# Kernel tuning notes

Hardware: AMD Instinct MI355X
Metric: run time of the kernel (lower is better)

## Reference

```python
import jax, jax.numpy as jnp
import numpy as np

DIM = 2048
HEADS = 16
DIM_HEAD = 128
FF_INNER = DIM * 4
SCALE_BASE = 512
EPS = 1e-5


def setup_inputs() -> dict:
    key = jax.random.key(0)
    k1, k2, k3, k4 = jax.random.split(key, 4)
    fused_out = HEADS * DIM_HEAD + DIM_HEAD + DIM_HEAD + 2 * FF_INNER  # 18688
    x = jax.random.normal(k1, (2, 2048, DIM), dtype=jnp.float32)
    gamma = jnp.ones((DIM,), dtype=jnp.float32)
    W_fused = jax.random.normal(k2, (DIM, fused_out), dtype=jnp.float32) * 0.02
    W_attn_out = jax.random.normal(k3, (HEADS * DIM_HEAD, DIM), dtype=jnp.float32) * 0.02
    W_ff_out = jax.random.normal(k4, (FF_INNER, DIM), dtype=jnp.float32) * 0.02
    return {"x": x, "gamma": gamma, "W_fused": W_fused, "W_attn_out": W_attn_out, "W_ff_out": W_ff_out}


def _rotate_half(t):
    t1, t2 = jnp.split(t, 2, axis=-1)
    return jnp.concatenate((-t2, t1), axis=-1)


def _rotary(n, dtype):
    # RotaryEmbedding with use_xpos=True, scale_base=512
    half = DIM_HEAD // 2
    inv_freq = 1.0 / (10000.0 ** (jnp.arange(0, DIM_HEAD, 2, dtype=dtype) / DIM_HEAD))
    t = jnp.arange(n, dtype=dtype)
    freqs = jnp.einsum('i,j->ij', t, inv_freq)          # [n, half]
    freqs = jnp.concatenate((freqs, freqs), axis=-1)    # [n, dh]
    scale_vec = (jnp.arange(0, DIM_HEAD, 2, dtype=dtype) + 0.4 * DIM_HEAD) / (1.4 * DIM_HEAD)
    power = (t - n // 2) / SCALE_BASE
    scale = scale_vec[None, :] ** power[:, None]        # [n, half]
    scale = jnp.concatenate((scale, scale), axis=-1)    # [n, dh]
    return freqs, scale


def _apply_rope(pos, t, scale):
    return t * jnp.cos(pos) * scale + _rotate_half(t) * jnp.sin(pos) * scale


def reference(x, gamma, W_fused, W_attn_out, W_ff_out):
    b, n, d = x.shape
    # LayerNorm (beta fixed at zero)
    mu = jnp.mean(x, axis=-1, keepdims=True)
    var = jnp.var(x, axis=-1, keepdims=True)
    xn = (x - mu) * jax.lax.rsqrt(var + EPS) * gamma

    proj = xn @ W_fused
    attn_inner = HEADS * DIM_HEAD
    q = proj[..., :attn_inner]
    k = proj[..., attn_inner:attn_inner + DIM_HEAD]
    v = proj[..., attn_inner + DIM_HEAD:attn_inner + 2 * DIM_HEAD]
    ff = proj[..., attn_inner + 2 * DIM_HEAD:]

    q = q.reshape(b, n, HEADS, DIM_HEAD).transpose(0, 2, 1, 3)  # b h n d

    pos, scale = _rotary(n, x.dtype)
    q = _apply_rope(pos, q, scale)            # broadcasts [n,dh] over b,h
    k = _apply_rope(pos, k, 1.0 / scale)      # k is [b, n, dh]

    # multi-query attention, causal
    sim = jnp.einsum('bhid,bjd->bhij', q, k) * (DIM_HEAD ** -0.5)
    causal_mask = jnp.triu(jnp.ones((n, n), dtype=bool), 1)
    sim = jnp.where(causal_mask, jnp.finfo(sim.dtype).min, sim)
    attn = jax.nn.softmax(sim, axis=-1)
    out = jnp.einsum('bhij,bjd->bhid', attn, v)
    out = out.transpose(0, 2, 1, 3).reshape(b, n, attn_inner)
    attn_out = out @ W_attn_out

    # SwiGLU: chunk -> silu(gate) * x
    ff_x, ff_gate = jnp.split(ff, 2, axis=-1)
    ff_out = (jax.nn.silu(ff_gate) * ff_x) @ W_ff_out

    return attn_out + ff_out
```

## Files before the change

### kernel.cpp

```cpp
#include <hip/hip_runtime.h>

typedef __attribute__((ext_vector_type(8))) short short8;
typedef __attribute__((ext_vector_type(4))) float floatx4;
typedef __attribute__((ext_vector_type(8))) unsigned short ushort8;

#define FOUT 18688
#define FFI  8192
#define CATW 10240

__device__ __forceinline__ float b2f(unsigned short u){
  union { unsigned int i; float f; } v; v.i = ((unsigned int)u) << 16; return v.f;
}
__device__ __forceinline__ unsigned short f2b(float f){
  union { float f; unsigned int i; } v; v.f = f;
  unsigned int r = v.i + 0x7FFFu + ((v.i >> 16) & 1u);
  return (unsigned short)(r >> 16);
}
__device__ __forceinline__ void gld_lds16(const void* g, void* l){
  __builtin_amdgcn_global_load_lds((const __attribute__((address_space(1))) void*)g,
                                   (__attribute__((address_space(3))) void*)l, 16, 0, 0);
}

#define SCHED0() __builtin_amdgcn_sched_barrier(0)
#define BARR()   do{ SCHED0(); __builtin_amdgcn_s_barrier(); SCHED0(); }while(0)

__global__ __launch_bounds__(256) void ln_kernel(const float* __restrict__ x,
                                                 const float* __restrict__ gamma,
                                                 unsigned short* __restrict__ xn){
  int row = blockIdx.x;
  const float* xr = x + (size_t)row * 2048;
  int tid = threadIdx.x;
  float v[8]; float s = 0.f, s2 = 0.f;
#pragma unroll
  for(int i=0;i<8;i++){ float t = xr[tid + i*256]; v[i]=t; s+=t; s2+=t*t; }
#pragma unroll
  for(int off=32; off>=1; off>>=1){ s += __shfl_down(s, off, 64); s2 += __shfl_down(s2, off, 64); }
  __shared__ float red[8];
  int wv = tid>>6, ln_ = tid&63;
  if(ln_==0){ red[wv] = s; red[wv+4] = s2; }
  __syncthreads();
  s  = red[0]+red[1]+red[2]+red[3];
  s2 = red[4]+red[5]+red[6]+red[7];
  float mu  = s * (1.f/2048.f);
  float var = s2 * (1.f/2048.f) - mu*mu;
  float rstd = rsqrtf(var + 1e-5f);
#pragma unroll
  for(int i=0;i<8;i++){
    float o = (v[i]-mu)*rstd*gamma[tid + i*256];
    xn[(size_t)row*2048 + tid + i*256] = f2b(o);
  }
}

__global__ __launch_bounds__(256) void tcast64_kernel(const float* __restrict__ W,
                                                      unsigned short* __restrict__ Wt,
                                                      int C, int S, int O){
  __shared__ float t[64][65];
  int bx = blockIdx.x*64;
  int by = blockIdx.y*64;
  int tid = threadIdx.x;
  int r = tid>>2, cq = (tid&3)*16;
  const float* src = W + (size_t)(by + r)*C + bx + cq;
#pragma unroll
  for(int e=0;e<4;e++){
    floatx4 v = *(const floatx4*)(src + e*4);
    t[r][cq+e*4+0]=v[0]; t[r][cq+e*4+1]=v[1]; t[r][cq+e*4+2]=v[2]; t[r][cq+e*4+3]=v[3];
  }
  __syncthreads();
#pragma unroll
  for(int it=0; it<2; it++){
    int s_ = it*256 + tid;
    int c = s_>>3, j8 = s_&7;
    ushort8 o;
#pragma unroll
    for(int e=0;e<8;e++) o[e] = f2b(t[j8*8+e][c]);
    *(ushort8*)&Wt[(size_t)(bx+c)*S + O + by + j8*8] = o;
  }
}

__global__ void vtrans_kernel(const unsigned short* __restrict__ proj, unsigned short* __restrict__ vt){
  __shared__ unsigned short t[32][33];
  int b = blockIdx.z;
  int n0 = blockIdx.x*32, d0 = blockIdx.y*32;
  int tx = threadIdx.x, ty = threadIdx.y;
#pragma unroll
  for(int i=0;i<4;i++) t[ty+i*8][tx] = proj[(size_t)(b*2048 + n0+ty+i*8)*FOUT + 2176 + d0+tx];
  __syncthreads();
#pragma unroll
  for(int i=0;i<4;i++) vt[((size_t)b*128 + d0+ty+i*8)*2048 + n0+tx] = t[tx][ty+i*8];
}

__global__ __launch_bounds__(256) void rope_tab_kernel(floatx4* __restrict__ tab){
  int idx = blockIdx.x*256 + threadIdx.x;
  int i = idx >> 6, j = idx & 63;
  float fj = (float)j, fi = (float)i;
  float p = fi * powf(10000.f, -fj*(1.f/64.f));
  float c = cosf(p), s = sinf(p);
  float sv = (2.f*fj + 51.2f) * (1.f/179.2f);
  float pw = (fi - 1024.f) * (1.f/512.f);
  float sc = powf(sv, pw);
  const float att = 0.08838834764831843f;
  floatx4 o; o[0]=c*sc*att; o[1]=s*sc*att; o[2]=c/sc; o[3]=s/sc;
  tab[idx] = o;
}

__global__ __launch_bounds__(256) void rope_kernel(unsigned short* __restrict__ proj,
                                                   const floatx4* __restrict__ tab){
  int row = blockIdx.x;
  int i = row & 2047;
  unsigned short* pr = proj + (size_t)row*FOUT;
  for(int item = threadIdx.x; item < 17*64; item += 256){
    int slot = item >> 6;
    int j = item & 63;
    floatx4 t = tab[i*64 + j];
    float cs = (slot==16) ? t[2] : t[0];
    float ss = (slot==16) ? t[3] : t[1];
    int colbase = (slot<16) ? slot*128 : 2048;
    float x1 = b2f(pr[colbase+j]);
    float x2 = b2f(pr[colbase+j+64]);
    pr[colbase+j]    = f2b(x1*cs - x2*ss);
    pr[colbase+j+64] = f2b(x2*cs + x1*ss);
  }
}

template<int MODE>
__global__ __launch_bounds__(512, 2) void gemm8p_kernel(const unsigned short* __restrict__ A,
                                                        const unsigned short* __restrict__ Bt,
                                                        unsigned short* __restrict__ Cb,
                                                        float* __restrict__ Cf,
                                                        int N, int K, int NT, size_t zstride){
  __shared__ unsigned short lds[65536];
  const int tid = threadIdx.x;
  const int wave = tid>>6, lane = tid&63;
  const int l15 = lane&15, l4 = lane>>4;
  const int wr = wave>>2, wc = wave&3;
  int id = blockIdx.x;
  int cpx = (int)gridDim.x >> 3;
  int swz = (id & 7)*cpx + (id >> 3);
  int tm = swz & 15, tn = swz >> 4;
  int kbase = (int)blockIdx.z * (NT*64);
  const unsigned short* Ab = A  + (size_t)tm*256*K + kbase;
  const unsigned short* Bb = Bt + (size_t)tn*256*K + kbase;
  if(MODE==1) Cf += (size_t)blockIdx.z * zstride;

  const int r0 = tid>>3;
  const int colc = ((tid&7) ^ (r0&7))*8;
  const int dstw = wave*512;

#define STAGE(t_, h_, isB_) do{ \
    const unsigned short* g_ = (isB_) ? Bb : Ab; \
    int db_ = (((t_)&1)<<15) + ((isB_)<<14) + ((h_)<<13) + dstw; \
    gld_lds16(g_ + (size_t)((h_)*128 + r0)*K + (t_)*64 + colc, &lds[db_]); \
    gld_lds16(g_ + (size_t)((h_)*128 + r0 + 64)*K + (t_)*64 + colc, &lds[db_ + 4096]); \
  }while(0)

  const int sw8 = l15&7;
  const int fo0 = ((l4    )^sw8)*8;
  const int fo1 = ((l4 + 4)^sw8)*8;
  const int albase = (wr*128 + l15)*64;
  const int blbase = 16384 + (wc*64 + l15)*64;

#define RD_A4(arr_, buf_, mh_, fo_) do{ \
  _Pragma("unroll") for(int mf=0; mf<4; mf++) \
    arr_[mf] = *(const short8*)&lds[(buf_) + albase + (mh_)*4096 + mf*1024 + (fo_)]; }while(0)
#define RD_B4(arr_, buf_, fo_) do{ \
  _Pragma("unroll") for(int nf=0; nf<4; nf++) \
    arr_[nf] = *(const short8*)&lds[(buf_) + blbase + nf*1024 + (fo_)]; }while(0)
#define MFMA_P(aarr_, barr_, mh_) do{ \
  _Pragma("unroll") for(int mf=0; mf<4; mf++) \
  _Pragma("unroll") for(int nf=0; nf<4; nf++) \
    acc[(mh_)*4+mf][nf] = __builtin_amdgcn_mfma_f32_16x16x32_bf16( \
      aarr_[mf], barr_[nf], acc[(mh_)*4+mf][nf], 0,0,0); }while(0)

  floatx4 acc[8][4];
#pragma unroll
  for(int i=0;i<8;i++)
#pragma unroll
    for(int j=0;j<4;j++) acc[i][j] = (floatx4)0.f;

  STAGE(0,0,0); STAGE(0,1,0); STAGE(0,0,1); STAGE(0,1,1);
  STAGE(1,0,1); STAGE(1,1,1); STAGE(1,0,0);
  asm volatile("s_waitcnt vmcnt(6)" ::: "memory");
  BARR();

  short8 a00_[4], a01_[4], a10_[4], a11_[4], b0_[4], b1_[4];
  for(int t=0; t<NT; ++t){
    const int bufo = (t&1)<<15;
    RD_A4(a00_, bufo, 0, fo0);
    RD_B4(b0_,  bufo, fo0);
    if(t+1 < NT) STAGE(t+1,1,0);
    __builtin_amdgcn_s_setprio(1);
    MFMA_P(a00_, b0_, 0);
    __builtin_amdgcn_s_setprio(0);
    BARR();
    RD_A4(a01_, bufo, 0, fo1);
    RD_B4(b1_,  bufo, fo1);
    if(t+2 < NT) STAGE(t+2,0,1);
    __builtin_amdgcn_s_setprio(1);
    MFMA_P(a01_, b1_, 0);
    __builtin_amdgcn_s_setprio(0);
    BARR();
    RD_A4(a10_, bufo, 1, fo0);
    if(t+2 < NT) STAGE(t+2,1,1);
    __builtin_amdgcn_s_setprio(1);
    MFMA_P(a10_, b0_, 1);
    __builtin_amdgcn_s_setprio(0);
    BARR();
    RD_A4(a11_, bufo, 1, fo1);
    if(t+2 < NT){
      STAGE(t+2,0,0);
      asm volatile("s_waitcnt vmcnt(6)" ::: "memory");
    } else if(t+1 < NT){
      asm volatile("s_waitcnt vmcnt(0)" ::: "memory");
    }
    __builtin_amdgcn_s_setprio(1);
    MFMA_P(a11_, b1_, 1);
    __builtin_amdgcn_s_setprio(0);
    BARR();
  }

#pragma unroll
  for(int m=0;m<8;m++){
#pragma unroll
    for(int n=0;n<4;n++){
#pragma unroll
      for(int r=0;r<4;r++){
        size_t row = (size_t)tm*256 + wr*128 + (m>>2)*64 + (m&3)*16 + l4*4 + r;
        size_t col = (size_t)tn*256 + wc*64 + n*16 + l15;
        float v = acc[m][n][r];
        if(MODE==0)      Cb[row*N + col] = f2b(v);
        else             Cf[row*N + col] = v;
      }
    }
  }
}

__global__ __launch_bounds__(256) void add2_kernel(const float* __restrict__ p0,
                                                   const float* __restrict__ p1,
                                                   float* __restrict__ o, int n4){
  for(int i = blockIdx.x*256 + threadIdx.x; i < n4; i += gridDim.x*256){
    floatx4 a = ((const floatx4*)p0)[i];
    floatx4 b = ((const floatx4*)p1)[i];
    ((floatx4*)o)[i] = a + b;
  }
}

__global__ __launch_bounds__(512) void attn_kernel(const unsigned short* __restrict__ proj,
                                                   const unsigned short* __restrict__ vt,
                                                   unsigned short* __restrict__ ao){
  __shared__ unsigned short lK[64*128];
  __shared__ unsigned short lV[128*64];
  __shared__ unsigned short lP[8*16*64];
  int qt = (int)gridDim.x - 1 - (int)blockIdx.x;
  int hh = blockIdx.y, b = blockIdx.z;
  int tid = threadIdx.x, wave = tid>>6, lane = tid&63;
  int l15 = lane&15, l4 = lane>>4;
  int q0 = qt*128;
  int qrow = q0 + wave*16 + l15;
  const unsigned short* qp = proj + (size_t)(b*2048 + qrow)*FOUT + hh*128 + l4*8;
  short8 qf[4];
#pragma unroll
  for(int ds=0; ds<4; ds++) qf[ds] = *(const short8*)(qp + ds*32);
  floatx4 po[8];
#pragma unroll
  for(int dt=0; dt<8; dt++) po[dt] = (floatx4)0.f;
  float mrun[4] = {-1e30f,-1e30f,-1e30f,-1e30f};
  float lrun[4] = {0.f,0.f,0.f,0.f};
  unsigned short* lPw = lP + wave*1024;
  const unsigned short* kb = proj + (size_t)(b*2048)*FOUT + 2048;
  const unsigned short* vb = vt + (size_t)b*128*2048;
  int kvmax = 2*qt + 1;

  for(int kv=0; kv<=kvmax; kv++){
    int kv0 = kv*64;
#pragma unroll
    for(int it=0; it<2; it++){
      int f = it*512 + tid;
      int r = f>>4, pc = f&15;
      int gc = pc ^ (r&7);
      gld_lds16(kb + (size_t)(kv0 + r)*FOUT + gc*8, &lK[(it*512 + wave*64)*8]);
    }
#pragma unroll
    for(int it=0; it<2; it++){
      int f = it*512 + tid;
      int d = f>>3, pc = f&7;
      int gc = pc ^ (d&7);
      gld_lds16(vb + (size_t)d*2048 + kv0 + gc*8, &lV[(it*512 + wave*64)*8]);
    }
    __syncthreads();
    floatx4 sa[4];
#pragma unroll
    for(int jt=0;jt<4;jt++) sa[jt] = (floatx4)0.f;
#pragma unroll
    for(int jt=0;jt<4;jt++){
      int krow = jt*16 + l15;
#pragma unroll
      for(int ds=0; ds<4; ds++){
        int pc = (l4 + ds*4) ^ (krow&7);
        short8 kf = *(const short8*)&lK[krow*128 + pc*8];
        sa[jt] = __builtin_amdgcn_mfma_f32_16x16x32_bf16(qf[ds], kf, sa[jt], 0,0,0);
      }
    }
    float pv[4][4];
    bool diag = (kv0 + 63 > q0 + wave*16);
#pragma unroll
    for(int jt=0;jt<4;jt++){
#pragma unroll
      for(int r=0;r<4;r++){
        float s = sa[jt][r];
        if(diag && (kv0 + jt*16 + l15 > q0 + wave*16 + l4*4 + r)) s = -1e30f;
        pv[jt][r] = s;
      }
    }
    float mnew[4], corr[4];
#pragma unroll
    for(int r=0;r<4;r++){
      float mx = fmaxf(fmaxf(pv[0][r],pv[1][r]),fmaxf(pv[2][r],pv[3][r]));
      mx = fmaxf(mx, __shfl_xor(mx, 1, 64));
      mx = fmaxf(mx, __shfl_xor(mx, 2, 64));
      mx = fmaxf(mx, __shfl_xor(mx, 4, 64));
      mx = fmaxf(mx, __shfl_xor(mx, 8, 64));
      float mn = fmaxf(mrun[r], mx);
      corr[r] = __expf(mrun[r] - mn);
      mrun[r] = mn;
      mnew[r] = mn;
    }
    float rsum[4] = {0.f,0.f,0.f,0.f};
#pragma unroll
    for(int jt=0;jt<4;jt++){
#pragma unroll
      for(int r=0;r<4;r++){
        float p = __expf(pv[jt][r] - mnew[r]);
        pv[jt][r] = p;
        rsum[r] += p;
      }
    }
#pragma unroll
    for(int r=0;r<4;r++){
      float rs = rsum[r];
      rs += __shfl_xor(rs, 1, 64);
      rs += __shfl_xor(rs, 2, 64);
      rs += __shfl_xor(rs, 4, 64);
      rs += __shfl_xor(rs, 8, 64);
      lrun[r] = lrun[r]*corr[r] + rs;
    }
#pragma unroll
    for(int dt=0;dt<8;dt++){
#pragma unroll
      for(int r=0;r<4;r++) po[dt][r] *= corr[r];
    }
#pragma unroll
    for(int jt=0;jt<4;jt++){
#pragma unroll
      for(int r=0;r<4;r++){
        int i_ = l4*4 + r;
        int j = jt*16 + l15;
        int pc = (j>>3) ^ (i_&7);
        lPw[i_*64 + pc*8 + (j&7)] = f2b(pv[jt][r]);
      }
    }
    asm volatile("s_waitcnt lgkmcnt(0)" ::: "memory");
    short8 pf[2];
#pragma unroll
    for(int ks=0;ks<2;ks++){
      int pc = (l4 + ks*4) ^ (l15&7);
      pf[ks] = *(const short8*)&lPw[l15*64 + pc*8];
    }
#pragma unroll
    for(int dt=0;dt<8;dt++){
      int d = dt*16 + l15;
#pragma unroll
      for(int ks=0;ks<2;ks++){
        int pc = (ks*4 + l4) ^ (d&7);
        short8 vf = *(const short8*)&lV[d*64 + pc*8];
        po[dt] = __builtin_amdgcn_mfma_f32_16x16x32_bf16(pf[ks], vf, po[dt], 0,0,0);
      }
    }
    __syncthreads();
  }
#pragma unroll
  for(int r=0;r<4;r++){
    float inv = 1.f / lrun[r];
    size_t orow = (size_t)(b*2048 + q0 + wave*16 + l4*4 + r);
#pragma unroll
    for(int dt=0;dt<8;dt++){
      ao[orow*CATW + hh*128 + dt*16 + l15] = f2b(po[dt][r]*inv);
    }
  }
}

__global__ __launch_bounds__(256) void swiglu_kernel(const unsigned short* __restrict__ proj,
                                                     unsigned short* __restrict__ cat){
  size_t idx = (size_t)blockIdx.x*256 + threadIdx.x;
  int row = (int)(idx >> 10);
  int c8  = (int)(idx & 1023);
  const unsigned short* pr = proj + (size_t)row*FOUT + 2304 + c8*8;
  ushort8 xv = *(const ushort8*)pr;
  ushort8 gv = *(const ushort8*)(pr + FFI);
  ushort8 ov;
#pragma unroll
  for(int e=0;e<8;e++){
    float xf = b2f(xv[e]);
    float gf = b2f(gv[e]);
    float sg = gf / (1.f + __expf(-gf));
    ov[e] = f2b(sg*xf);
  }
  *(ushort8*)(cat + (size_t)row*CATW + 2048 + c8*8) = ov;
}

extern "C" void kernel_launch(void* const* d_in, const int* in_sizes, int n_in,
                              void* d_out, int out_size, void* d_ws, size_t ws_size,
                              hipStream_t stream){
  const float* x     = (const float*)d_in[0];
  const float* gamma = (const float*)d_in[1];
  const float* Wf    = (const float*)d_in[2];
  const float* Wa    = (const float*)d_in[3];
  const float* Wff   = (const float*)d_in[4];
  float* out = (float*)d_out;

  char* p = (char*)d_ws;
  unsigned short* xn    = (unsigned short*)p;  p += (size_t)4096*2048*2;
  unsigned short* WfT   = (unsigned short*)p;  p += (size_t)18688*2048*2;
  unsigned short* proj  = (unsigned short*)p;  p += (size_t)4096*18688*2;
  unsigned short* BtCat = (unsigned short*)p;  p += (size_t)2048*CATW*2;
  unsigned short* cat   = (unsigned short*)p;  p += (size_t)4096*CATW*2;
  unsigned short* vtb   = (unsigned short*)p;  p += (size_t)2*128*2048*2;
  floatx4*        rtab  = (floatx4*)p;         p += (size_t)2048*64*16;
  float* part = (float*)d_ws;

  ln_kernel<<<4096, 256, 0, stream>>>(x, gamma, xn);
  rope_tab_kernel<<<512, 256, 0, stream>>>(rtab);
  tcast64_kernel<<<dim3(292,32),  256, 0, stream>>>(Wf,  WfT,   18688, 2048, 0);
  tcast64_kernel<<<dim3(32,32),   256, 0, stream>>>(Wa,  BtCat, 2048,  CATW, 0);
  tcast64_kernel<<<dim3(32,128),  256, 0, stream>>>(Wff, BtCat, 2048,  CATW, 2048);
  gemm8p_kernel<0><<<dim3(1168,1,1), 512, 0, stream>>>(xn, WfT, proj, nullptr, 18688, 2048, 32, 0);
  rope_kernel<<<4096, 256, 0, stream>>>(proj, rtab);
  vtrans_kernel<<<dim3(64,4,2), dim3(32,8), 0, stream>>>(proj, vtb);
  attn_kernel<<<dim3(16,16,2), 512, 0, stream>>>(proj, vtb, cat);
  swiglu_kernel<<<16384, 256, 0, stream>>>(proj, cat);
  gemm8p_kernel<1><<<dim3(128,1,2), 512, 0, stream>>>(cat, BtCat, nullptr, part, 2048, 10240, 80,
                                                      (size_t)4096*2048);
  add2_kernel<<<2048, 256, 0, stream>>>(part, part + (size_t)4096*2048, out, 2097152);
}
```

Before: 741.4 us.

## Halve GEMM barriers per k-step and raise output GEMM split-K to four

The GEMM main loop now issues the LDS reads for both k-halves before the first barrier and all three next-tile stages together, so each k-iteration needs two barriers instead of four. The vmcnt wait moves to the end of the iteration. The output-projection GEMM now uses four K-splits instead of two, giving 512 workgroups instead of 256 to fill the CUs. A new add4 kernel sums the four partial buffers. The trade-off is more partial-sum traffic, higher register pressure from holding more fragments at once, and possible LDS hazards or workspace overlap from the reordered staging and the larger partial buffer.

```diff
diff --git a/kernel.cpp b/kernel.cpp
--- a/kernel.cpp
+++ b/kernel.cpp
@@ -187,34 +187,23 @@
     const int bufo = (t&1)<<15;
     RD_A4(a00_, bufo, 0, fo0);
     RD_B4(b0_,  bufo, fo0);
+    RD_A4(a01_, bufo, 0, fo1);
+    RD_B4(b1_,  bufo, fo1);
     if(t+1 < NT) STAGE(t+1,1,0);
     __builtin_amdgcn_s_setprio(1);
     MFMA_P(a00_, b0_, 0);
-    __builtin_amdgcn_s_setprio(0);
-    BARR();
-    RD_A4(a01_, bufo, 0, fo1);
-    RD_B4(b1_,  bufo, fo1);
-    if(t+2 < NT) STAGE(t+2,0,1);
-    __builtin_amdgcn_s_setprio(1);
     MFMA_P(a01_, b1_, 0);
     __builtin_amdgcn_s_setprio(0);
     BARR();
     RD_A4(a10_, bufo, 1, fo0);
-    if(t+2 < NT) STAGE(t+2,1,1);
+    RD_A4(a11_, bufo, 1, fo1);
+    if(t+2 < NT){ STAGE(t+2,0,1); STAGE(t+2,1,1); STAGE(t+2,0,0); }
     __builtin_amdgcn_s_setprio(1);
     MFMA_P(a10_, b0_, 1);
-    __builtin_amdgcn_s_setprio(0);
-    BARR();
-    RD_A4(a11_, bufo, 1, fo1);
-    if(t+2 < NT){
-      STAGE(t+2,0,0);
-      asm volatile("s_waitcnt vmcnt(6)" ::: "memory");
-    } else if(t+1 < NT){
-      asm volatile("s_waitcnt vmcnt(0)" ::: "memory");
-    }
-    __builtin_amdgcn_s_setprio(1);
     MFMA_P(a11_, b1_, 1);
     __builtin_amdgcn_s_setprio(0);
+    if(t+2 < NT){      asm volatile("s_waitcnt vmcnt(6)" ::: "memory"); }
+    else if(t+1 < NT){ asm volatile("s_waitcnt vmcnt(0)" ::: "memory"); }
     BARR();
   }
 
@@ -234,13 +223,14 @@
   }
 }
 
-__global__ __launch_bounds__(256) void add2_kernel(const float* __restrict__ p0,
-                                                   const float* __restrict__ p1,
+__global__ __launch_bounds__(256) void add4_kernel(const float* __restrict__ pp,
                                                    float* __restrict__ o, int n4){
+  const floatx4* p0 = (const floatx4*)pp;
+  const floatx4* p1 = p0 + 2097152;
+  const floatx4* p2 = p1 + 2097152;
+  const floatx4* p3 = p2 + 2097152;
   for(int i = blockIdx.x*256 + threadIdx.x; i < n4; i += gridDim.x*256){
-    floatx4 a = ((const floatx4*)p0)[i];
-    floatx4 b = ((const floatx4*)p1)[i];
-    ((floatx4*)o)[i] = a + b;
+    ((floatx4*)o)[i] = (p0[i] + p1[i]) + (p2[i] + p3[i]);
   }
 }
 
@@ -437,7 +427,7 @@
   vtrans_kernel<<<dim3(64,4,2), dim3(32,8), 0, stream>>>(proj, vtb);
   attn_kernel<<<dim3(16,16,2), 512, 0, stream>>>(proj, vtb, cat);
   swiglu_kernel<<<16384, 256, 0, stream>>>(proj, cat);
-  gemm8p_kernel<1><<<dim3(128,1,2), 512, 0, stream>>>(cat, BtCat, nullptr, part, 2048, 10240, 80,
+  gemm8p_kernel<1><<<dim3(128,1,4), 512, 0, stream>>>(cat, BtCat, nullptr, part, 2048, 10240, 40,
                                                       (size_t)4096*2048);
-  add2_kernel<<<2048, 256, 0, stream>>>(part, part + (size_t)4096*2048, out, 2097152);
-}
+  add4_kernel<<<2048, 256, 0, stream>>>(part, out, 2097152);
+}
```

New measurement: 766.4 us. 3.4% more time.

## Replace 256x256 8-wave GEMM with simpler 128x256 4-wave double-buffered GEMM

Applied to the files above, without the earlier changes.

Swaps the hand-pipelined 512-thread GEMM that used 256x256 tiles, K-step 64 and sub-phase barriers for a 256-thread kernel with 128x256 tiles and K-step 32. The new kernel uses a plain double buffer with a full vmcnt(0) wait per iteration and drops the XOR LDS swizzle. It halves LDS use so more blocks can fit per CU. The cost is lower arithmetic intensity, more global loads per FLOP, possible LDS bank conflicts and less overlap of loads with MFMA.

```diff
diff --git a/kernel.cpp b/kernel.cpp
--- a/kernel.cpp
+++ b/kernel.cpp
@@ -123,110 +123,75 @@
 }
 
 template<int MODE>
-__global__ __launch_bounds__(512, 2) void gemm8p_kernel(const unsigned short* __restrict__ A,
+__global__ __launch_bounds__(256, 2) void gemm2b_kernel(const unsigned short* __restrict__ A,
                                                         const unsigned short* __restrict__ Bt,
                                                         unsigned short* __restrict__ Cb,
                                                         float* __restrict__ Cf,
                                                         int N, int K, int NT, size_t zstride){
-  __shared__ unsigned short lds[65536];
+  __shared__ unsigned short lds[24576];
   const int tid = threadIdx.x;
   const int wave = tid>>6, lane = tid&63;
   const int l15 = lane&15, l4 = lane>>4;
-  const int wr = wave>>2, wc = wave&3;
   int id = blockIdx.x;
   int cpx = (int)gridDim.x >> 3;
   int swz = (id & 7)*cpx + (id >> 3);
-  int tm = swz & 15, tn = swz >> 4;
-  int kbase = (int)blockIdx.z * (NT*64);
-  const unsigned short* Ab = A  + (size_t)tm*256*K + kbase;
+  int tm = swz & 31, tn = swz >> 5;
+  int kbase = (int)blockIdx.z * (NT*32);
+  const unsigned short* Ab = A  + (size_t)tm*128*K + kbase;
   const unsigned short* Bb = Bt + (size_t)tn*256*K + kbase;
   if(MODE==1) Cf += (size_t)blockIdx.z * zstride;
 
-  const int r0 = tid>>3;
-  const int colc = ((tid&7) ^ (r0&7))*8;
+  const int r0 = tid>>2;
+  const int colc = (tid&3)*8;
   const int dstw = wave*512;
 
-#define STAGE(t_, h_, isB_) do{ \
-    const unsigned short* g_ = (isB_) ? Bb : Ab; \
-    int db_ = (((t_)&1)<<15) + ((isB_)<<14) + ((h_)<<13) + dstw; \
-    gld_lds16(g_ + (size_t)((h_)*128 + r0)*K + (t_)*64 + colc, &lds[db_]); \
-    gld_lds16(g_ + (size_t)((h_)*128 + r0 + 64)*K + (t_)*64 + colc, &lds[db_ + 4096]); \
+#define STG(t_, bufo_) do{ \
+    gld_lds16(Ab + (size_t)(r0     )*K + (t_)*32 + colc, &lds[(bufo_) + dstw]); \
+    gld_lds16(Ab + (size_t)(r0 + 64)*K + (t_)*32 + colc, &lds[(bufo_) + 2048 + dstw]); \
+    _Pragma("unroll") for(int j_=0; j_<4; j_++) \
+      gld_lds16(Bb + (size_t)(r0 + j_*64)*K + (t_)*32 + colc, &lds[(bufo_) + 4096 + j_*2048 + dstw]); \
   }while(0)
 
-  const int sw8 = l15&7;
-  const int fo0 = ((l4    )^sw8)*8;
-  const int fo1 = ((l4 + 4)^sw8)*8;
-  const int albase = (wr*128 + l15)*64;
-  const int blbase = 16384 + (wc*64 + l15)*64;
-
-#define RD_A4(arr_, buf_, mh_, fo_) do{ \
-  _Pragma("unroll") for(int mf=0; mf<4; mf++) \
-    arr_[mf] = *(const short8*)&lds[(buf_) + albase + (mh_)*4096 + mf*1024 + (fo_)]; }while(0)
-#define RD_B4(arr_, buf_, fo_) do{ \
-  _Pragma("unroll") for(int nf=0; nf<4; nf++) \
-    arr_[nf] = *(const short8*)&lds[(buf_) + blbase + nf*1024 + (fo_)]; }while(0)
-#define MFMA_P(aarr_, barr_, mh_) do{ \
-  _Pragma("unroll") for(int mf=0; mf<4; mf++) \
-  _Pragma("unroll") for(int nf=0; nf<4; nf++) \
-    acc[(mh_)*4+mf][nf] = __builtin_amdgcn_mfma_f32_16x16x32_bf16( \
-      aarr_[mf], barr_[nf], acc[(mh_)*4+mf][nf], 0,0,0); }while(0)
-
   floatx4 acc[8][4];
 #pragma unroll
   for(int i=0;i<8;i++)
 #pragma unroll
     for(int j=0;j<4;j++) acc[i][j] = (floatx4)0.f;
 
-  STAGE(0,0,0); STAGE(0,1,0); STAGE(0,0,1); STAGE(0,1,1);
-  STAGE(1,0,1); STAGE(1,1,1); STAGE(1,0,0);
-  asm volatile("s_waitcnt vmcnt(6)" ::: "memory");
+  STG(0, 0);
+  asm volatile("s_waitcnt vmcnt(0)" ::: "memory");
   BARR();
 
-  short8 a00_[4], a01_[4], a10_[4], a11_[4], b0_[4], b1_[4];
+  short8 a_[8], b_[4];
   for(int t=0; t<NT; ++t){
-    const int bufo = (t&1)<<15;
-    RD_A4(a00_, bufo, 0, fo0);
-    RD_B4(b0_,  bufo, fo0);
-    if(t+1 < NT) STAGE(t+1,1,0);
+    const int bufo = (t&1)*12288;
+#pragma unroll
+    for(int mf=0; mf<8; mf++)
+      a_[mf] = *(const short8*)&lds[bufo + (mf*16 + l15)*32 + l4*8];
+#pragma unroll
+    for(int nf=0; nf<4; nf++)
+      b_[nf] = *(const short8*)&lds[bufo + 4096 + (wave*64 + nf*16 + l15)*32 + l4*8];
+    if(t+1 < NT) STG(t+1, bufo ^ 12288);
     __builtin_amdgcn_s_setprio(1);
-    MFMA_P(a00_, b0_, 0);
+#pragma unroll
+    for(int mf=0; mf<8; mf++)
+#pragma unroll
+      for(int nf=0; nf<4; nf++)
+        acc[mf][nf] = __builtin_amdgcn_mfma_f32_16x16x32_bf16(a_[mf], b_[nf], acc[mf][nf], 0,0,0);
     __builtin_amdgcn_s_setprio(0);
+    if(t+1 < NT){ asm volatile("s_waitcnt vmcnt(0)" ::: "memory"); }
     BARR();
-    RD_A4(a01_, bufo, 0, fo1);
-    RD_B4(b1_,  bufo, fo1);
-    if(t+2 < NT) STAGE(t+2,0,1);
-    __builtin_amdgcn_s_setprio(1);
-    MFMA_P(a01_, b1_, 0);
-    __builtin_amdgcn_s_setprio(0);
-    BARR();
-    RD_A4(a10_, bufo, 1, fo0);
-    if(t+2 < NT) STAGE(t+2,1,1);
-    __builtin_amdgcn_s_setprio(1);
-    MFMA_P(a10_, b0_, 1);
-    __builtin_amdgcn_s_setprio(0);
-    BARR();
-    RD_A4(a11_, bufo, 1, fo1);
-    if(t+2 < NT){
-      STAGE(t+2,0,0);
-      asm volatile("s_waitcnt vmcnt(6)" ::: "memory");
-    } else if(t+1 < NT){
-      asm volatile("s_waitcnt vmcnt(0)" ::: "memory");
-    }
-    __builtin_amdgcn_s_setprio(1);
-    MFMA_P(a11_, b1_, 1);
-    __builtin_amdgcn_s_setprio(0);
-    BARR();
-  }
-
-#pragma unroll
-  for(int m=0;m<8;m++){
-#pragma unroll
-    for(int n=0;n<4;n++){
-#pragma unroll
-      for(int r=0;r<4;r++){
-        size_t row = (size_t)tm*256 + wr*128 + (m>>2)*64 + (m&3)*16 + l4*4 + r;
-        size_t col = (size_t)tn*256 + wc*64 + n*16 + l15;
-        float v = acc[m][n][r];
+  }
+
+#pragma unroll
+  for(int mf=0; mf<8; mf++){
+#pragma unroll
+    for(int nf=0; nf<4; nf++){
+#pragma unroll
+      for(int r=0; r<4; r++){
+        size_t row = (size_t)tm*128 + mf*16 + l4*4 + r;
+        size_t col = (size_t)tn*256 + wave*64 + nf*16 + l15;
+        float v = acc[mf][nf][r];
         if(MODE==0)      Cb[row*N + col] = f2b(v);
         else             Cf[row*N + col] = v;
       }
@@ -432,12 +397,12 @@
   tcast64_kernel<<<dim3(292,32),  256, 0, stream>>>(Wf,  WfT,   18688, 2048, 0);
   tcast64_kernel<<<dim3(32,32),   256, 0, stream>>>(Wa,  BtCat, 2048,  CATW, 0);
   tcast64_kernel<<<dim3(32,128),  256, 0, stream>>>(Wff, BtCat, 2048,  CATW, 2048);
-  gemm8p_kernel<0><<<dim3(1168,1,1), 512, 0, stream>>>(xn, WfT, proj, nullptr, 18688, 2048, 32, 0);
+  gemm2b_kernel<0><<<dim3(2336,1,1), 256, 0, stream>>>(xn, WfT, proj, nullptr, 18688, 2048, 64, 0);
   rope_kernel<<<4096, 256, 0, stream>>>(proj, rtab);
   vtrans_kernel<<<dim3(64,4,2), dim3(32,8), 0, stream>>>(proj, vtb);
   attn_kernel<<<dim3(16,16,2), 512, 0, stream>>>(proj, vtb, cat);
   swiglu_kernel<<<16384, 256, 0, stream>>>(proj, cat);
-  gemm8p_kernel<1><<<dim3(128,1,2), 512, 0, stream>>>(cat, BtCat, nullptr, part, 2048, 10240, 80,
+  gemm2b_kernel<1><<<dim3(256,1,2), 256, 0, stream>>>(cat, BtCat, nullptr, part, 2048, 10240, 160,
                                                       (size_t)4096*2048);
   add2_kernel<<<2048, 256, 0, stream>>>(part, part + (size_t)4096*2048, out, 2097152);
 }
```

New measurement: 872.9 us. 1.18x slower.

## Double-buffer K/V tiles in attention kernel to overlap loads with compute

Applied to the files above, without the earlier changes.

The attention kernel now keeps two LDS buffers for K and V. It issues the global-to-LDS loads for the next KV tile right after the barrier, so they run while the current tile is being computed. The trailing barrier is removed, leaving one sync per iteration preceded by a vmcnt wait. This roughly doubles K/V shared memory, which may reduce occupancy, and correctness depends on the single barrier ordering buffer reuse properly.

```diff
diff --git a/kernel.cpp b/kernel.cpp
--- a/kernel.cpp
+++ b/kernel.cpp
@@ -247,9 +247,9 @@
 __global__ __launch_bounds__(512) void attn_kernel(const unsigned short* __restrict__ proj,
                                                    const unsigned short* __restrict__ vt,
                                                    unsigned short* __restrict__ ao){
-  __shared__ unsigned short lK[64*128];
-  __shared__ unsigned short lV[128*64];
-  __shared__ unsigned short lP[8*16*64];
+  __shared__ unsigned short lK[2*8192];
+  __shared__ unsigned short lV[2*8192];
+  __shared__ unsigned short lP[8*1024];
   int qt = (int)gridDim.x - 1 - (int)blockIdx.x;
   int hh = blockIdx.y, b = blockIdx.z;
   int tid = threadIdx.x, wave = tid>>6, lane = tid&63;
@@ -270,23 +270,29 @@
   const unsigned short* vb = vt + (size_t)b*128*2048;
   int kvmax = 2*qt + 1;
 
+#define STAGE_K(kv_, bo_) do{ \
+    _Pragma("unroll") for(int it=0; it<2; it++){ \
+      int f = it*512 + tid; \
+      int r = f>>4, pc = f&15; \
+      int gc = pc ^ (r&7); \
+      gld_lds16(kb + (size_t)((kv_)*64 + r)*FOUT + gc*8, &lK[(bo_) + (it*512 + wave*64)*8]); \
+    } }while(0)
+#define STAGE_V(kv_, bo_) do{ \
+    _Pragma("unroll") for(int it=0; it<2; it++){ \
+      int f = it*512 + tid; \
+      int d = f>>3, pc = f&7; \
+      int gc = pc ^ (d&7); \
+      gld_lds16(vb + (size_t)d*2048 + (kv_)*64 + gc*8, &lV[(bo_) + (it*512 + wave*64)*8]); \
+    } }while(0)
+
+  STAGE_K(0, 0); STAGE_V(0, 0);
+
   for(int kv=0; kv<=kvmax; kv++){
     int kv0 = kv*64;
-#pragma unroll
-    for(int it=0; it<2; it++){
-      int f = it*512 + tid;
-      int r = f>>4, pc = f&15;
-      int gc = pc ^ (r&7);
-      gld_lds16(kb + (size_t)(kv0 + r)*FOUT + gc*8, &lK[(it*512 + wave*64)*8]);
-    }
-#pragma unroll
-    for(int it=0; it<2; it++){
-      int f = it*512 + tid;
-      int d = f>>3, pc = f&7;
-      int gc = pc ^ (d&7);
-      gld_lds16(vb + (size_t)d*2048 + kv0 + gc*8, &lV[(it*512 + wave*64)*8]);
-    }
+    int cb = (kv&1)*8192;
+    asm volatile("s_waitcnt vmcnt(0)" ::: "memory");
     __syncthreads();
+    if(kv < kvmax){ STAGE_K(kv+1, cb^8192); STAGE_V(kv+1, cb^8192); }
     floatx4 sa[4];
 #pragma unroll
     for(int jt=0;jt<4;jt++) sa[jt] = (floatx4)0.f;
@@ -296,7 +302,7 @@
 #pragma unroll
       for(int ds=0; ds<4; ds++){
         int pc = (l4 + ds*4) ^ (krow&7);
-        short8 kf = *(const short8*)&lK[krow*128 + pc*8];
+        short8 kf = *(const short8*)&lK[cb + krow*128 + pc*8];
         sa[jt] = __builtin_amdgcn_mfma_f32_16x16x32_bf16(qf[ds], kf, sa[jt], 0,0,0);
       }
     }
@@ -371,11 +377,10 @@
 #pragma unroll
       for(int ks=0;ks<2;ks++){
         int pc = (ks*4 + l4) ^ (d&7);
-        short8 vf = *(const short8*)&lV[d*64 + pc*8];
+        short8 vf = *(const short8*)&lV[cb + d*64 + pc*8];
         po[dt] = __builtin_amdgcn_mfma_f32_16x16x32_bf16(pf[ks], vf, po[dt], 0,0,0);
       }
     }
-    __syncthreads();
   }
 #pragma unroll
   for(int r=0;r<4;r++){
```

Result: no change. 734.2 us, median of 2 (-1.0%).
